# Performance work log

Hardware: AMD Instinct MI355X
Metric: run time of the kernel (lower is better)

Reference implementation:

```python
import jax, jax.numpy as jnp
import numpy as np

DIM = 1024
NUM_HEADS = 16
HEAD_DIM = DIM // NUM_HEADS
SCALE = HEAD_DIM ** -0.5


def setup_inputs() -> dict:
    key = jax.random.key(0)
    k1, k2, k3 = jax.random.split(key, 3)
    x = jax.random.normal(k1, (2, 2048, DIM), dtype=jnp.float32)
    # nn.Linear weights: stored as [out, in]; y = x @ W.T
    w_qkv = jax.random.normal(k2, (3 * DIM, DIM), dtype=jnp.float32) * (DIM ** -0.5)
    w_proj = jax.random.normal(k3, (DIM, DIM), dtype=jnp.float32) * (DIM ** -0.5)
    return {"x": x, "w_qkv": w_qkv, "w_proj": w_proj}


def reference(x, w_qkv, w_proj):
    B, L, D = x.shape
    qkv = jnp.einsum("bld,ed->ble", x, w_qkv)  # [B, L, 3*D]
    qkv = qkv.reshape(B, L, 3, NUM_HEADS, HEAD_DIM).transpose(2, 0, 3, 1, 4)
    q, k, v = qkv[0], qkv[1], qkv[2]  # each [B, H, L, hd]
    attn = jnp.einsum("bhqd,bhkd->bhqk", q, k) * SCALE
    attn = jax.nn.softmax(attn, axis=-1)
    out = jnp.einsum("bhqk,bhkd->bhqd", attn, v)  # [B, H, L, hd]
    out = out.transpose(0, 2, 1, 3).reshape(B, L, D)
    return jnp.einsum("bld,ed->ble", out, w_proj)
```

## Files before the change

### kernel.cpp

```cpp
#include <hip/hip_runtime.h>
#include <math.h>
#include <stdint.h>

#define B_ 2
#define L_ 2048
#define D_ 1024
#define H_ 16
#define HD_ 64
#define QSCALE_ 0.1803368801f

typedef __attribute__((ext_vector_type(8))) short short8;
typedef __attribute__((ext_vector_type(4))) short short4v;
typedef __attribute__((ext_vector_type(4))) float float4v;

#if defined(__has_builtin)
#if __has_builtin(__builtin_amdgcn_exp2f)
#define EXP2F(x) __builtin_amdgcn_exp2f(x)
#endif
#endif
#ifndef EXP2F
#define EXP2F(x) exp2f(x)
#endif

__device__ __forceinline__ short f2bf(float f) {
    union { float f; unsigned u; } x; x.f = f;
    unsigned r = x.u + 0x7fffu + ((x.u >> 16) & 1u);
    return (short)(r >> 16);
}

__device__ __forceinline__ unsigned fbits(float f) {
    union { float f; unsigned u; } x; x.f = f;
    return x.u;
}

__device__ __forceinline__ unsigned pk_bf_trunc(float a, float b) {
    return __builtin_amdgcn_perm(fbits(b), fbits(a), 0x07060302u);
}

__global__ __launch_bounds__(256) void cvt_all(const float* __restrict__ x,
                                               const float* __restrict__ wqkv,
                                               const float* __restrict__ wproj,
                                               short* __restrict__ xb,
                                               short* __restrict__ wqkvb,
                                               short* __restrict__ wprojb) {
    int i = blockIdx.x * 256 + threadIdx.x;
    const float* in;
    short* out;
    int idx;
    if (i < 1048576)      { in = x;     out = xb;     idx = i; }
    else if (i < 1835008) { in = wqkv;  out = wqkvb;  idx = i - 1048576; }
    else                  { in = wproj; out = wprojb; idx = i - 1835008; }
    float4 v = ((const float4*)in)[idx];
    short4v o;
    o.x = f2bf(v.x); o.y = f2bf(v.y); o.z = f2bf(v.z); o.w = f2bf(v.w);
    ((short4v*)out)[idx] = o;
}

__global__ __launch_bounds__(256) void gemm_qkv_bf16(const short* __restrict__ A,
                                                     const short* __restrict__ Bm,
                                                     short* __restrict__ Qb,
                                                     short* __restrict__ Kb,
                                                     short* __restrict__ Vb) {
    __shared__ short smem[16384];
    const int tid = threadIdx.x;
    const int w = tid >> 6, l = tid & 63;
    const int lm = l & 15, q = l >> 4;
    const int bid = blockIdx.x;
    const int xcd = bid & 7;
    const int grp = bid >> 3;
    const int n_tile = xcd + 8 * (grp % 3);
    const int m_tile = grp / 3;
    const int m0 = m_tile * 128, n0 = n_tile * 128;
    const int wm = w >> 1, wn = w & 1;

    const int srow = tid >> 2;
    const int sc8  = (tid & 3) * 8;
    const int soff0 = srow * 32 + sc8;
    const int soff1 = soff0 + 64 * 32;
    const short* Ag = A  + (size_t)(m0 + srow) * 1024 + sc8;
    const short* Bg = Bm + (size_t)(n0 + srow) * 1024 + sc8;

    float4v acc[4][4];
#pragma unroll
    for (int mt = 0; mt < 4; ++mt)
#pragma unroll
        for (int nt = 0; nt < 4; ++nt) acc[mt][nt] = (float4v){0.f, 0.f, 0.f, 0.f};

    {
        short8 a0 = *(const short8*)(Ag);
        short8 a1 = *(const short8*)(Ag + 64 * 1024);
        short8 b0 = *(const short8*)(Bg);
        short8 b1 = *(const short8*)(Bg + 64 * 1024);
        *(short8*)(smem + soff0) = a0;
        *(short8*)(smem + soff1) = a1;
        *(short8*)(smem + 8192 + soff0) = b0;
        *(short8*)(smem + 8192 + soff1) = b1;
    }
    short8 ar0 = *(const short8*)(Ag + 32);
    short8 ar1 = *(const short8*)(Ag + 64 * 1024 + 32);
    short8 br0 = *(const short8*)(Bg + 32);
    short8 br1 = *(const short8*)(Bg + 64 * 1024 + 32);

    for (int t = 0; t < 32; ++t) {
        const int cur = t & 1;
        short* Asc = smem + cur * 4096;
        short* Asn = smem + (1 - cur) * 4096;
        short* Bsc = smem + 8192 + cur * 4096;
        short* Bsn = smem + 8192 + (1 - cur) * 4096;

        __syncthreads();

        if (t < 31) {
            *(short8*)(Asn + soff0) = ar0;
            *(short8*)(Asn + soff1) = ar1;
            *(short8*)(Bsn + soff0) = br0;
            *(short8*)(Bsn + soff1) = br1;
        }
        if (t < 30) {
            const int k0 = (t + 2) * 32;
            ar0 = *(const short8*)(Ag + k0);
            ar1 = *(const short8*)(Ag + 64 * 1024 + k0);
            br0 = *(const short8*)(Bg + k0);
            br1 = *(const short8*)(Bg + 64 * 1024 + k0);
        }

        short8 af[4], bfr[4];
#pragma unroll
        for (int mt = 0; mt < 4; ++mt)
            af[mt] = *(const short8*)(Asc + (wm * 64 + mt * 16 + lm) * 32 + q * 8);
#pragma unroll
        for (int nt = 0; nt < 4; ++nt)
            bfr[nt] = *(const short8*)(Bsc + (wn * 64 + nt * 16 + lm) * 32 + q * 8);
#pragma unroll
        for (int mt = 0; mt < 4; ++mt)
#pragma unroll
            for (int nt = 0; nt < 4; ++nt)
                acc[mt][nt] = __builtin_amdgcn_mfma_f32_16x16x32_bf16(af[mt], bfr[nt], acc[mt][nt], 0, 0, 0);
    }

    const int which = n0 >> 10;
    if (which < 2) {
        short* dst = (which == 0) ? Qb : Kb;
        const float sc = (which == 0) ? QSCALE_ : 1.0f;
#pragma unroll
        for (int half = 0; half < 2; ++half) {
            __syncthreads();
            if (wm == half) {
#pragma unroll
                for (int mt = 0; mt < 4; ++mt)
#pragma unroll
                    for (int nt = 0; nt < 4; ++nt)
#pragma unroll
                        for (int r = 0; r < 4; ++r)
                            smem[(mt * 16 + q * 4 + r) * 128 + wn * 64 + nt * 16 + lm] =
                                f2bf(acc[mt][nt][r] * sc);
            }
            __syncthreads();
#pragma unroll
            for (int j = 0; j < 4; ++j) {
                const int x = tid + 256 * j;
                const int row = x >> 4, c = x & 15;
                short8 v = *(const short8*)(smem + row * 128 + c * 8);
                const int m = m0 + half * 64 + row;
                const int b = m >> 11, ll = m & 2047;
                const int n = n0 + c * 8;
                const int hh = (n & 1023) >> 6, d = n & 63;
                *(short8*)(dst + (((size_t)b * H_ + hh) * L_ + ll) * HD_ + d) = v;
            }
        }
    } else {
        const int mbase = m0 + wm * 64;
        const int b = mbase >> 11;
        const int llb = (mbase & 2047);
#pragma unroll
        for (int mt = 0; mt < 4; ++mt) {
            const int ll = llb + (mt >> 1) * 32 + q * 8 + (mt & 1) * 4;
#pragma unroll
            for (int nt = 0; nt < 4; ++nt) {
                const int n = n0 + wn * 64 + nt * 16 + lm;
                const int h = (n & 1023) >> 6, d = n & 63;
                short4v pk;
                pk.x = f2bf(acc[mt][nt][0]); pk.y = f2bf(acc[mt][nt][1]);
                pk.z = f2bf(acc[mt][nt][2]); pk.w = f2bf(acc[mt][nt][3]);
                *(short4v*)(Vb + (((size_t)b * H_ + h) * HD_ + d) * L_ + ll) = pk;
            }
        }
    }
}

__global__ __launch_bounds__(256) void attn_mfma(const short* __restrict__ Qb,
                                                 const short* __restrict__ Kb,
                                                 const short* __restrict__ Vtg,
                                                 short* __restrict__ Ob) {
    __shared__ short KV[4 * 4096];

    const int tid = threadIdx.x;
    const int w = tid >> 6, l = tid & 63;
    const int lm = l & 15, q = l >> 4;
    const int bid = blockIdx.x;
    const int grp = bid >> 3;
    const int bh = (bid & 7) * 4 + (grp & 3);
    const int qt = grp >> 2;

    const short* Qg = Qb  + ((size_t)bh * L_ + qt * 128) * HD_;
    const short* Kg = Kb  + (size_t)bh * L_ * HD_;
    const short* Vg = Vtg + (size_t)bh * HD_ * L_;

    short* Qs = KV + 8192;
#pragma unroll
    for (int t = 0; t < 4; ++t) {
        int idx = tid + 256 * t;
        int row = idx >> 3, c = idx & 7;
        short8 v = *(const short8*)(Qg + row * 64 + c * 8);
        *(short8*)(Qs + row * 64 + ((c ^ (row & 7)) * 8)) = v;
    }

    const int srow = tid >> 3;
    const int sc   = tid & 7;
    const int koff0 = srow * 64 + ((sc ^ (srow & 7)) * 8);
    const int koff1 = koff0 + 32 * 64;

    {
        short8 ka = *(const short8*)(Kg + (size_t)srow * 64 + sc * 8);
        short8 kb = *(const short8*)(Kg + (size_t)(srow + 32) * 64 + sc * 8);
        short8 va = *(const short8*)(Vg + (size_t)srow * L_ + sc * 8);
        short8 vb = *(const short8*)(Vg + (size_t)(srow + 32) * L_ + sc * 8);
        *(short8*)(KV + koff0) = ka;
        *(short8*)(KV + koff1) = kb;
        *(short8*)(KV + 4096 + koff0) = va;
        *(short8*)(KV + 4096 + koff1) = vb;
    }
    short8 kra = *(const short8*)(Kg + (size_t)(64 + srow) * 64 + sc * 8);
    short8 krb = *(const short8*)(Kg + (size_t)(64 + srow + 32) * 64 + sc * 8);
    short8 vra = *(const short8*)(Vg + (size_t)srow * L_ + 64 + sc * 8);
    short8 vrb = *(const short8*)(Vg + (size_t)(srow + 32) * L_ + 64 + sc * 8);

    __syncthreads();

    short8 qf[2][2];
#pragma unroll
    for (int nq = 0; nq < 2; ++nq)
#pragma unroll
        for (int kh = 0; kh < 2; ++kh) {
            int row = w * 32 + nq * 16 + lm;
            int ch = kh * 4 + q;
            qf[nq][kh] = *(const short8*)(Qs + row * 64 + ((ch ^ (row & 7)) * 8));
        }

    int offA0[4], offA1[4], offV[2][4];
#pragma unroll
    for (int nt = 0; nt < 4; ++nt) {
        const int arow = nt * 16 + lm;
        offA0[nt] = arow * 64 + ((q ^ (arow & 7)) * 8);
        offA1[nt] = arow * 64 + (((4 + q) ^ (arow & 7)) * 8);
#pragma unroll
        for (int kh = 0; kh < 2; ++kh)
            offV[kh][nt] = arow * 64 + (((kh * 4 + q) ^ (arow & 7)) * 8);
    }

    float4v o[4][2];
#pragma unroll
    for (int mt = 0; mt < 4; ++mt)
#pragma unroll
        for (int nq = 0; nq < 2; ++nq) o[mt][nq] = (float4v){0.f, 0.f, 0.f, 0.f};
    float lsum[2] = {0.f, 0.f};

#pragma unroll 2
    for (int t = 0; t < 32; ++t) {
        const int cur = t & 1;
        short* Kl = KV + cur * 8192;
        short* Vt = Kl + 4096;
        short* Kn = KV + (1 - cur) * 8192;
        short* Vn = Kn + 4096;

        __syncthreads();

        if (t < 31) {
            *(short8*)(Kn + koff0) = kra;
            *(short8*)(Kn + koff1) = krb;
            *(short8*)(Vn + koff0) = vra;
            *(short8*)(Vn + koff1) = vrb;
        }
        if (t < 30) {
            kra = *(const short8*)(Kg + (size_t)((t + 2) * 64 + srow) * 64 + sc * 8);
            krb = *(const short8*)(Kg + (size_t)((t + 2) * 64 + srow + 32) * 64 + sc * 8);
            vra = *(const short8*)(Vg + (size_t)srow * L_ + (t + 2) * 64 + sc * 8);
            vrb = *(const short8*)(Vg + (size_t)(srow + 32) * L_ + (t + 2) * 64 + sc * 8);
        }

        float4v st[4][2];
#pragma unroll
        for (int nt = 0; nt < 4; ++nt) {
            short8 a0 = *(const short8*)(Kl + offA0[nt]);
            short8 a1 = *(const short8*)(Kl + offA1[nt]);
#pragma unroll
            for (int nq = 0; nq < 2; ++nq) {
                float4v z = (float4v){0.f, 0.f, 0.f, 0.f};
                z = __builtin_amdgcn_mfma_f32_16x16x32_bf16(a0, qf[nq][0], z, 0, 0, 0);
                z = __builtin_amdgcn_mfma_f32_16x16x32_bf16(a1, qf[nq][1], z, 0, 0, 0);
                st[nt][nq] = z;
            }
        }

        short8 pb[2][2];
#pragma unroll
        for (int nq = 0; nq < 2; ++nq) {
            float e[4][4];
#pragma unroll
            for (int nt = 0; nt < 4; ++nt) {
                e[nt][0] = EXP2F(st[nt][nq][0]);
                e[nt][1] = EXP2F(st[nt][nq][1]);
                e[nt][2] = EXP2F(st[nt][nq][2]);
                e[nt][3] = EXP2F(st[nt][nq][3]);
                lsum[nq] += (e[nt][0] + e[nt][1]) + (e[nt][2] + e[nt][3]);
            }
            union { short8 s8; unsigned u[4]; } p0, p1;
            p0.u[0] = pk_bf_trunc(e[0][0], e[0][1]);
            p0.u[1] = pk_bf_trunc(e[0][2], e[0][3]);
            p0.u[2] = pk_bf_trunc(e[1][0], e[1][1]);
            p0.u[3] = pk_bf_trunc(e[1][2], e[1][3]);
            p1.u[0] = pk_bf_trunc(e[2][0], e[2][1]);
            p1.u[1] = pk_bf_trunc(e[2][2], e[2][3]);
            p1.u[2] = pk_bf_trunc(e[3][0], e[3][1]);
            p1.u[3] = pk_bf_trunc(e[3][2], e[3][3]);
            pb[0][nq] = p0.s8;
            pb[1][nq] = p1.s8;
        }

#pragma unroll
        for (int kh = 0; kh < 2; ++kh)
#pragma unroll
            for (int mt = 0; mt < 4; ++mt) {
                short8 va = *(const short8*)(Vt + offV[kh][mt]);
#pragma unroll
                for (int nq = 0; nq < 2; ++nq)
                    o[mt][nq] = __builtin_amdgcn_mfma_f32_16x16x32_bf16(va, pb[kh][nq], o[mt][nq], 0, 0, 0);
            }
    }

    float inv[2];
#pragma unroll
    for (int nq = 0; nq < 2; ++nq) {
        float s = lsum[nq];
        s += __shfl_xor(s, 16);
        s += __shfl_xor(s, 32);
        inv[nq] = 1.f / s;
    }
    short* OgBase = Ob + ((size_t)bh * L_ + qt * 128) * HD_;
#pragma unroll
    for (int nq = 0; nq < 2; ++nq) {
        const int qrow = w * 32 + nq * 16 + lm;
#pragma unroll
        for (int mt = 0; mt < 4; ++mt) {
            short4v pk;
            pk.x = f2bf(o[mt][nq][0] * inv[nq]);
            pk.y = f2bf(o[mt][nq][1] * inv[nq]);
            pk.z = f2bf(o[mt][nq][2] * inv[nq]);
            pk.w = f2bf(o[mt][nq][3] * inv[nq]);
            *(short4v*)(OgBase + (size_t)qrow * 64 + mt * 16 + q * 4) = pk;
        }
    }
}

__global__ __launch_bounds__(256) void gemm_proj_bf16(const short* __restrict__ Ob,
                                                      const short* __restrict__ Wp,
                                                      float* __restrict__ out) {
    __shared__ short As[2 * 2048];
    __shared__ short Bs[2 * 4096];
    const int tid = threadIdx.x;
    const int w = tid >> 6, l = tid & 63;
    const int lm = l & 15, q = l >> 4;
    const int bid = blockIdx.x;
    const int m0 = (bid >> 3) * 64, n0 = (bid & 7) * 128;
    const int wm = w & 1, wn = w >> 1;
    const int b = m0 >> 11, l0 = m0 & 2047;

    const int srow = tid >> 2;
    const int sc8  = (tid & 3) * 8;
    const int aoff = srow * 32 + sc8;
    const int boff0 = aoff;
    const int boff1 = aoff + 64 * 32;
    const short* Agb = Ob + (((size_t)b * H_) * L_ + l0 + srow) * HD_;
    const short* Bg  = Wp + (size_t)(n0 + srow) * 1024 + sc8;

    float4v acc[2][4];
#pragma unroll
    for (int mt = 0; mt < 2; ++mt)
#pragma unroll
        for (int nt = 0; nt < 4; ++nt) acc[mt][nt] = (float4v){0.f, 0.f, 0.f, 0.f};

    {
        short8 a0 = *(const short8*)(Agb + sc8);
        short8 b0 = *(const short8*)(Bg);
        short8 b1 = *(const short8*)(Bg + 64 * 1024);
        *(short8*)(As + aoff) = a0;
        *(short8*)(Bs + boff0) = b0;
        *(short8*)(Bs + boff1) = b1;
    }
    short8 arx = *(const short8*)(Agb + 32 + sc8);
    short8 brx0 = *(const short8*)(Bg + 32);
    short8 brx1 = *(const short8*)(Bg + 64 * 1024 + 32);

    for (int t = 0; t < 32; ++t) {
        const int cur = t & 1;
        short* Asc = As + cur * 2048;
        short* Asn = As + (1 - cur) * 2048;
        short* Bsc = Bs + cur * 4096;
        short* Bsn = Bs + (1 - cur) * 4096;

        __syncthreads();

        if (t < 31) {
            *(short8*)(Asn + aoff) = arx;
            *(short8*)(Bsn + boff0) = brx0;
            *(short8*)(Bsn + boff1) = brx1;
        }
        if (t < 30) {
            const int tn = t + 2;
            const int hh = tn >> 1, d = (tn & 1) * 32 + sc8;
            arx  = *(const short8*)(Agb + (size_t)hh * L_ * HD_ + d);
            brx0 = *(const short8*)(Bg + tn * 32);
            brx1 = *(const short8*)(Bg + 64 * 1024 + tn * 32);
        }

        short8 af[2], bfr[4];
#pragma unroll
        for (int mt = 0; mt < 2; ++mt)
            af[mt] = *(const short8*)(Asc + (wm * 32 + mt * 16 + lm) * 32 + q * 8);
#pragma unroll
        for (int nt = 0; nt < 4; ++nt)
            bfr[nt] = *(const short8*)(Bsc + (wn * 64 + nt * 16 + lm) * 32 + q * 8);
#pragma unroll
        for (int mt = 0; mt < 2; ++mt)
#pragma unroll
            for (int nt = 0; nt < 4; ++nt)
                acc[mt][nt] = __builtin_amdgcn_mfma_f32_16x16x32_bf16(af[mt], bfr[nt], acc[mt][nt], 0, 0, 0);
    }

#pragma unroll
    for (int mt = 0; mt < 2; ++mt)
#pragma unroll
        for (int nt = 0; nt < 4; ++nt)
#pragma unroll
            for (int r = 0; r < 4; ++r) {
                const int m = m0 + wm * 32 + mt * 16 + q * 4 + r;
                const int n = n0 + wn * 64 + nt * 16 + lm;
                out[(size_t)m * 1024 + n] = acc[mt][nt][r];
            }
}

extern "C" void kernel_launch(void* const* d_in, const int* in_sizes, int n_in,
                              void* d_out, int out_size, void* d_ws, size_t ws_size,
                              hipStream_t stream) {
    (void)in_sizes; (void)n_in; (void)out_size; (void)ws_size;
    const float* x      = (const float*)d_in[0];
    const float* w_qkv  = (const float*)d_in[1];
    const float* w_proj = (const float*)d_in[2];

    char* ws = (char*)d_ws;
    short* xb     = (short*)(ws);
    short* wqkvb  = (short*)(ws + (8u  << 20));
    short* wprojb = (short*)(ws + (14u << 20));
    short* Qb     = (short*)(ws + (16u << 20));
    short* Kb     = (short*)(ws + (24u << 20));
    short* Vb     = (short*)(ws + (32u << 20));
    short* Ob     = (short*)(ws + (40u << 20));

    cvt_all<<<8192, 256, 0, stream>>>(x, w_qkv, w_proj, xb, wqkvb, wprojb);
    gemm_qkv_bf16 <<<768, 256, 0, stream>>>(xb, wqkvb, Qb, Kb, Vb);
    attn_mfma     <<<512, 256, 0, stream>>>(Qb, Kb, Vb, Ob);
    gemm_proj_bf16<<<512, 256, 0, stream>>>(Ob, wprojb, (float*)d_out);
}
```

Baseline: 171.8 us.

## Use direct global-to-LDS loads for GEMM tile staging in QKV and proj kernels

Replaces the register-staged double-buffered global loads in both GEMM kernels with global_load_lds DMA copies straight into shared memory. Each wave now fills its own contiguous LDS slice, and the loop issues the next stage's loads before computing on the current buffer, with one barrier per iteration. The aim is to save the VGPRs and the VALU/LDS write instructions used for staging. The cost is a one-stage prefetch distance instead of two, and it depends on the intrinsic's per-wave LDS layout matching the fragment reads.

```diff
diff --git a/kernel.cpp b/kernel.cpp
--- a/kernel.cpp
+++ b/kernel.cpp
@@ -35,6 +35,12 @@
 
 __device__ __forceinline__ unsigned pk_bf_trunc(float a, float b) {
     return __builtin_amdgcn_perm(fbits(b), fbits(a), 0x07060302u);
+}
+
+__device__ __forceinline__ void gl16(const short* g, short* l) {
+    __builtin_amdgcn_global_load_lds((const __attribute__((address_space(1))) void*)g,
+                                     (__attribute__((address_space(3))) void*)l,
+                                     16, 0, 0);
 }
 
 __global__ __launch_bounds__(256) void cvt_all(const float* __restrict__ x,
@@ -73,12 +79,21 @@
     const int m0 = m_tile * 128, n0 = n_tile * 128;
     const int wm = w >> 1, wn = w & 1;
 
-    const int srow = tid >> 2;
-    const int sc8  = (tid & 3) * 8;
-    const int soff0 = srow * 32 + sc8;
-    const int soff1 = soff0 + 64 * 32;
-    const short* Ag = A  + (size_t)(m0 + srow) * 1024 + sc8;
-    const short* Bg = Bm + (size_t)(n0 + srow) * 1024 + sc8;
+    const int lrow = l >> 2;
+    const int lcol = (l & 3) * 8;
+    const short* Ag0 = A  + (size_t)(m0 + w * 32 + lrow) * 1024 + lcol;
+    const short* Bg0 = Bm + (size_t)(n0 + w * 32 + lrow) * 1024 + lcol;
+    short* AsL = smem + w * 1024;
+    short* BsL = smem + 8192 + w * 1024;
+
+#define STAGE_QKV(T, C) { \
+        const int ko_ = (T) * 32; \
+        short* al_ = AsL + (C) * 4096; \
+        short* bl_ = BsL + (C) * 4096; \
+        gl16(Ag0 + ko_, al_); \
+        gl16(Ag0 + 16 * 1024 + ko_, al_ + 512); \
+        gl16(Bg0 + ko_, bl_); \
+        gl16(Bg0 + 16 * 1024 + ko_, bl_ + 512); }
 
     float4v acc[4][4];
 #pragma unroll
@@ -86,44 +101,15 @@
 #pragma unroll
         for (int nt = 0; nt < 4; ++nt) acc[mt][nt] = (float4v){0.f, 0.f, 0.f, 0.f};
 
-    {
-        short8 a0 = *(const short8*)(Ag);
-        short8 a1 = *(const short8*)(Ag + 64 * 1024);
-        short8 b0 = *(const short8*)(Bg);
-        short8 b1 = *(const short8*)(Bg + 64 * 1024);
-        *(short8*)(smem + soff0) = a0;
-        *(short8*)(smem + soff1) = a1;
-        *(short8*)(smem + 8192 + soff0) = b0;
-        *(short8*)(smem + 8192 + soff1) = b1;
-    }
-    short8 ar0 = *(const short8*)(Ag + 32);
-    short8 ar1 = *(const short8*)(Ag + 64 * 1024 + 32);
-    short8 br0 = *(const short8*)(Bg + 32);
-    short8 br1 = *(const short8*)(Bg + 64 * 1024 + 32);
+    STAGE_QKV(0, 0);
+    __syncthreads();
 
     for (int t = 0; t < 32; ++t) {
         const int cur = t & 1;
-        short* Asc = smem + cur * 4096;
-        short* Asn = smem + (1 - cur) * 4096;
-        short* Bsc = smem + 8192 + cur * 4096;
-        short* Bsn = smem + 8192 + (1 - cur) * 4096;
-
-        __syncthreads();
-
-        if (t < 31) {
-            *(short8*)(Asn + soff0) = ar0;
-            *(short8*)(Asn + soff1) = ar1;
-            *(short8*)(Bsn + soff0) = br0;
-            *(short8*)(Bsn + soff1) = br1;
-        }
-        if (t < 30) {
-            const int k0 = (t + 2) * 32;
-            ar0 = *(const short8*)(Ag + k0);
-            ar1 = *(const short8*)(Ag + 64 * 1024 + k0);
-            br0 = *(const short8*)(Bg + k0);
-            br1 = *(const short8*)(Bg + 64 * 1024 + k0);
-        }
-
+        if (t < 31) STAGE_QKV(t + 1, cur ^ 1);
+
+        const short* Asc = smem + cur * 4096;
+        const short* Bsc = smem + 8192 + cur * 4096;
         short8 af[4], bfr[4];
 #pragma unroll
         for (int mt = 0; mt < 4; ++mt)
@@ -136,7 +122,10 @@
 #pragma unroll
             for (int nt = 0; nt < 4; ++nt)
                 acc[mt][nt] = __builtin_amdgcn_mfma_f32_16x16x32_bf16(af[mt], bfr[nt], acc[mt][nt], 0, 0, 0);
-    }
+
+        if (t < 31) __syncthreads();
+    }
+#undef STAGE_QKV
 
     const int which = n0 >> 10;
     if (which < 2) {
@@ -375,13 +364,18 @@
     const int wm = w & 1, wn = w >> 1;
     const int b = m0 >> 11, l0 = m0 & 2047;
 
-    const int srow = tid >> 2;
-    const int sc8  = (tid & 3) * 8;
-    const int aoff = srow * 32 + sc8;
-    const int boff0 = aoff;
-    const int boff1 = aoff + 64 * 32;
-    const short* Agb = Ob + (((size_t)b * H_) * L_ + l0 + srow) * HD_;
-    const short* Bg  = Wp + (size_t)(n0 + srow) * 1024 + sc8;
+    const int lrow = l >> 2;
+    const int lcol = (l & 3) * 8;
+    const short* Abase = Ob + ((size_t)b * H_) * L_ * HD_ + (size_t)(l0 + w * 16 + lrow) * HD_;
+    const short* Bg0 = Wp + (size_t)(n0 + w * 32 + lrow) * 1024 + lcol;
+    short* AsL = As + w * 512;
+    short* BsL = Bs + w * 1024;
+
+#define STAGE_PROJ(T, C) { \
+        gl16(Abase + (size_t)((T) >> 1) * L_ * HD_ + (((T) & 1) * 32 + lcol), AsL + (C) * 2048); \
+        const int ko_ = (T) * 32; \
+        gl16(Bg0 + ko_, BsL + (C) * 4096); \
+        gl16(Bg0 + 16 * 1024 + ko_, BsL + (C) * 4096 + 512); }
 
     float4v acc[2][4];
 #pragma unroll
@@ -389,40 +383,15 @@
 #pragma unroll
         for (int nt = 0; nt < 4; ++nt) acc[mt][nt] = (float4v){0.f, 0.f, 0.f, 0.f};
 
-    {
-        short8 a0 = *(const short8*)(Agb + sc8);
-        short8 b0 = *(const short8*)(Bg);
-        short8 b1 = *(const short8*)(Bg + 64 * 1024);
-        *(short8*)(As + aoff) = a0;
-        *(short8*)(Bs + boff0) = b0;
-        *(short8*)(Bs + boff1) = b1;
-    }
-    short8 arx = *(const short8*)(Agb + 32 + sc8);
-    short8 brx0 = *(const short8*)(Bg + 32);
-    short8 brx1 = *(const short8*)(Bg + 64 * 1024 + 32);
+    STAGE_PROJ(0, 0);
+    __syncthreads();
 
     for (int t = 0; t < 32; ++t) {
         const int cur = t & 1;
-        short* Asc = As + cur * 2048;
-        short* Asn = As + (1 - cur) * 2048;
-        short* Bsc = Bs + cur * 4096;
-        short* Bsn = Bs + (1 - cur) * 4096;
-
-        __syncthreads();
-
-        if (t < 31) {
-            *(short8*)(Asn + aoff) = arx;
-            *(short8*)(Bsn + boff0) = brx0;
-            *(short8*)(Bsn + boff1) = brx1;
-        }
-        if (t < 30) {
-            const int tn = t + 2;
-            const int hh = tn >> 1, d = (tn & 1) * 32 + sc8;
-            arx  = *(const short8*)(Agb + (size_t)hh * L_ * HD_ + d);
-            brx0 = *(const short8*)(Bg + tn * 32);
-            brx1 = *(const short8*)(Bg + 64 * 1024 + tn * 32);
-        }
-
+        if (t < 31) STAGE_PROJ(t + 1, cur ^ 1);
+
+        const short* Asc = As + cur * 2048;
+        const short* Bsc = Bs + cur * 4096;
         short8 af[2], bfr[4];
 #pragma unroll
         for (int mt = 0; mt < 2; ++mt)
@@ -435,7 +404,10 @@
 #pragma unroll
             for (int nt = 0; nt < 4; ++nt)
                 acc[mt][nt] = __builtin_amdgcn_mfma_f32_16x16x32_bf16(af[mt], bfr[nt], acc[mt][nt], 0, 0, 0);
-    }
+
+        if (t < 31) __syncthreads();
+    }
+#undef STAGE_PROJ
 
 #pragma unroll
     for (int mt = 0; mt < 2; ++mt)
```

After: 178.9 us. +4.1%, slower.

## Use 8 waves per attention block with 16 query rows per wave

Applied to the files above, without the earlier changes.

The attention kernel now launches 512 threads per block instead of 256. Each of the 8 waves handles 16 query rows instead of 32, and each thread loads one K/V chunk per tile instead of two. This halves per-wave register state (accumulators, score tiles, Q fragments), which can raise occupancy and latency hiding. In exchange, each K/V fragment read from LDS now feeds only one MFMA rather than two, so LDS traffic per flop doubles, and block-wide barriers span more waves.

```diff
diff --git a/kernel.cpp b/kernel.cpp
--- a/kernel.cpp
+++ b/kernel.cpp
@@ -188,7 +188,7 @@
     }
 }
 
-__global__ __launch_bounds__(256) void attn_mfma(const short* __restrict__ Qb,
+__global__ __launch_bounds__(512) void attn_mfma(const short* __restrict__ Qb,
                                                  const short* __restrict__ Kb,
                                                  const short* __restrict__ Vtg,
                                                  short* __restrict__ Ob) {
@@ -208,8 +208,8 @@
 
     short* Qs = KV + 8192;
 #pragma unroll
-    for (int t = 0; t < 4; ++t) {
-        int idx = tid + 256 * t;
+    for (int t = 0; t < 2; ++t) {
+        int idx = tid + 512 * t;
         int row = idx >> 3, c = idx & 7;
         short8 v = *(const short8*)(Qg + row * 64 + c * 8);
         *(short8*)(Qs + row * 64 + ((c ^ (row & 7)) * 8)) = v;
@@ -217,35 +217,26 @@
 
     const int srow = tid >> 3;
     const int sc   = tid & 7;
-    const int koff0 = srow * 64 + ((sc ^ (srow & 7)) * 8);
-    const int koff1 = koff0 + 32 * 64;
+    const int koff = srow * 64 + ((sc ^ (srow & 7)) * 8);
 
     {
         short8 ka = *(const short8*)(Kg + (size_t)srow * 64 + sc * 8);
-        short8 kb = *(const short8*)(Kg + (size_t)(srow + 32) * 64 + sc * 8);
         short8 va = *(const short8*)(Vg + (size_t)srow * L_ + sc * 8);
-        short8 vb = *(const short8*)(Vg + (size_t)(srow + 32) * L_ + sc * 8);
-        *(short8*)(KV + koff0) = ka;
-        *(short8*)(KV + koff1) = kb;
-        *(short8*)(KV + 4096 + koff0) = va;
-        *(short8*)(KV + 4096 + koff1) = vb;
+        *(short8*)(KV + koff) = ka;
+        *(short8*)(KV + 4096 + koff) = va;
     }
     short8 kra = *(const short8*)(Kg + (size_t)(64 + srow) * 64 + sc * 8);
-    short8 krb = *(const short8*)(Kg + (size_t)(64 + srow + 32) * 64 + sc * 8);
     short8 vra = *(const short8*)(Vg + (size_t)srow * L_ + 64 + sc * 8);
-    short8 vrb = *(const short8*)(Vg + (size_t)(srow + 32) * L_ + 64 + sc * 8);
 
     __syncthreads();
 
-    short8 qf[2][2];
-#pragma unroll
-    for (int nq = 0; nq < 2; ++nq)
-#pragma unroll
-        for (int kh = 0; kh < 2; ++kh) {
-            int row = w * 32 + nq * 16 + lm;
-            int ch = kh * 4 + q;
-            qf[nq][kh] = *(const short8*)(Qs + row * 64 + ((ch ^ (row & 7)) * 8));
-        }
+    short8 qf[2];
+#pragma unroll
+    for (int kh = 0; kh < 2; ++kh) {
+        int row = w * 16 + lm;
+        int ch = kh * 4 + q;
+        qf[kh] = *(const short8*)(Qs + row * 64 + ((ch ^ (row & 7)) * 8));
+    }
 
     int offA0[4], offA1[4], offV[2][4];
 #pragma unroll
@@ -258,12 +249,10 @@
             offV[kh][nt] = arow * 64 + (((kh * 4 + q) ^ (arow & 7)) * 8);
     }
 
-    float4v o[4][2];
-#pragma unroll
-    for (int mt = 0; mt < 4; ++mt)
-#pragma unroll
-        for (int nq = 0; nq < 2; ++nq) o[mt][nq] = (float4v){0.f, 0.f, 0.f, 0.f};
-    float lsum[2] = {0.f, 0.f};
+    float4v o[4];
+#pragma unroll
+    for (int mt = 0; mt < 4; ++mt) o[mt] = (float4v){0.f, 0.f, 0.f, 0.f};
+    float lsum = 0.f;
 
 #pragma unroll 2
     for (int t = 0; t < 32; ++t) {
@@ -276,44 +265,36 @@
         __syncthreads();
 
         if (t < 31) {
-            *(short8*)(Kn + koff0) = kra;
-            *(short8*)(Kn + koff1) = krb;
-            *(short8*)(Vn + koff0) = vra;
-            *(short8*)(Vn + koff1) = vrb;
+            *(short8*)(Kn + koff) = kra;
+            *(short8*)(Vn + koff) = vra;
         }
         if (t < 30) {
             kra = *(const short8*)(Kg + (size_t)((t + 2) * 64 + srow) * 64 + sc * 8);
-            krb = *(const short8*)(Kg + (size_t)((t + 2) * 64 + srow + 32) * 64 + sc * 8);
             vra = *(const short8*)(Vg + (size_t)srow * L_ + (t + 2) * 64 + sc * 8);
-            vrb = *(const short8*)(Vg + (size_t)(srow + 32) * L_ + (t + 2) * 64 + sc * 8);
-        }
-
-        float4v st[4][2];
+        }
+
+        float4v st[4];
 #pragma unroll
         for (int nt = 0; nt < 4; ++nt) {
             short8 a0 = *(const short8*)(Kl + offA0[nt]);
             short8 a1 = *(const short8*)(Kl + offA1[nt]);
-#pragma unroll
-            for (int nq = 0; nq < 2; ++nq) {
-                float4v z = (float4v){0.f, 0.f, 0.f, 0.f};
-                z = __builtin_amdgcn_mfma_f32_16x16x32_bf16(a0, qf[nq][0], z, 0, 0, 0);
-                z = __builtin_amdgcn_mfma_f32_16x16x32_bf16(a1, qf[nq][1], z, 0, 0, 0);
-                st[nt][nq] = z;
-            }
-        }
-
-        short8 pb[2][2];
-#pragma unroll
-        for (int nq = 0; nq < 2; ++nq) {
-            float e[4][4];
-#pragma unroll
-            for (int nt = 0; nt < 4; ++nt) {
-                e[nt][0] = EXP2F(st[nt][nq][0]);
-                e[nt][1] = EXP2F(st[nt][nq][1]);
-                e[nt][2] = EXP2F(st[nt][nq][2]);
-                e[nt][3] = EXP2F(st[nt][nq][3]);
-                lsum[nq] += (e[nt][0] + e[nt][1]) + (e[nt][2] + e[nt][3]);
-            }
+            float4v z = (float4v){0.f, 0.f, 0.f, 0.f};
+            z = __builtin_amdgcn_mfma_f32_16x16x32_bf16(a0, qf[0], z, 0, 0, 0);
+            z = __builtin_amdgcn_mfma_f32_16x16x32_bf16(a1, qf[1], z, 0, 0, 0);
+            st[nt] = z;
+        }
+
+        float e[4][4];
+#pragma unroll
+        for (int nt = 0; nt < 4; ++nt) {
+            e[nt][0] = EXP2F(st[nt][0]);
+            e[nt][1] = EXP2F(st[nt][1]);
+            e[nt][2] = EXP2F(st[nt][2]);
+            e[nt][3] = EXP2F(st[nt][3]);
+            lsum += (e[nt][0] + e[nt][1]) + (e[nt][2] + e[nt][3]);
+        }
+        short8 pb[2];
+        {
             union { short8 s8; unsigned u[4]; } p0, p1;
             p0.u[0] = pk_bf_trunc(e[0][0], e[0][1]);
             p0.u[1] = pk_bf_trunc(e[0][2], e[0][3]);
@@ -323,8 +304,8 @@
             p1.u[1] = pk_bf_trunc(e[2][2], e[2][3]);
             p1.u[2] = pk_bf_trunc(e[3][0], e[3][1]);
             p1.u[3] = pk_bf_trunc(e[3][2], e[3][3]);
-            pb[0][nq] = p0.s8;
-            pb[1][nq] = p1.s8;
+            pb[0] = p0.s8;
+            pb[1] = p1.s8;
         }
 
 #pragma unroll
@@ -332,33 +313,24 @@
 #pragma unroll
             for (int mt = 0; mt < 4; ++mt) {
                 short8 va = *(const short8*)(Vt + offV[kh][mt]);
-#pragma unroll
-                for (int nq = 0; nq < 2; ++nq)
-                    o[mt][nq] = __builtin_amdgcn_mfma_f32_16x16x32_bf16(va, pb[kh][nq], o[mt][nq], 0, 0, 0);
+                o[mt] = __builtin_amdgcn_mfma_f32_16x16x32_bf16(va, pb[kh], o[mt], 0, 0, 0);
             }
     }
 
-    float inv[2];
-#pragma unroll
-    for (int nq = 0; nq < 2; ++nq) {
-        float s = lsum[nq];
-        s += __shfl_xor(s, 16);
-        s += __shfl_xor(s, 32);
-        inv[nq] = 1.f / s;
-    }
+    float s = lsum;
+    s += __shfl_xor(s, 16);
+    s += __shfl_xor(s, 32);
+    const float inv = 1.f / s;
     short* OgBase = Ob + ((size_t)bh * L_ + qt * 128) * HD_;
-#pragma unroll
-    for (int nq = 0; nq < 2; ++nq) {
-        const int qrow = w * 32 + nq * 16 + lm;
-#pragma unroll
-        for (int mt = 0; mt < 4; ++mt) {
-            short4v pk;
-            pk.x = f2bf(o[mt][nq][0] * inv[nq]);
-            pk.y = f2bf(o[mt][nq][1] * inv[nq]);
-            pk.z = f2bf(o[mt][nq][2] * inv[nq]);
-            pk.w = f2bf(o[mt][nq][3] * inv[nq]);
-            *(short4v*)(OgBase + (size_t)qrow * 64 + mt * 16 + q * 4) = pk;
-        }
+    const int qrow = w * 16 + lm;
+#pragma unroll
+    for (int mt = 0; mt < 4; ++mt) {
+        short4v pk;
+        pk.x = f2bf(o[mt][0] * inv);
+        pk.y = f2bf(o[mt][1] * inv);
+        pk.z = f2bf(o[mt][2] * inv);
+        pk.w = f2bf(o[mt][3] * inv);
+        *(short4v*)(OgBase + (size_t)qrow * 64 + mt * 16 + q * 4) = pk;
     }
 }
 
@@ -468,6 +440,6 @@
 
     cvt_all<<<8192, 256, 0, stream>>>(x, w_qkv, w_proj, xb, wqkvb, wprojb);
     gemm_qkv_bf16 <<<768, 256, 0, stream>>>(xb, wqkvb, Qb, Kb, Vb);
-    attn_mfma     <<<512, 256, 0, stream>>>(Qb, Kb, Vb, Ob);
+    attn_mfma     <<<512, 512, 0, stream>>>(Qb, Kb, Vb, Ob);
     gemm_proj_bf16<<<512, 256, 0, stream>>>(Ob, wprojb, (float*)d_out);
 }
```

Measured after the change: 174.4 us. About the same (+1.5%).
